# Performance work log

Hardware: AMD Instinct MI355X
Metric: run time of the kernel (lower is better)

## Reference

```python
import jax, jax.numpy as jnp
import numpy as np

B, S, D = 2, 4096, 768
H = 12
HD = D // H  # 64


def setup_inputs() -> dict:
    key = jax.random.key(0)
    ks = jax.random.split(key, 6)
    scale = 0.02
    return {
        "x": jax.random.normal(ks[0], (B, S, D), dtype=jnp.float32),
        "w_query": jax.random.normal(ks[1], (D, D), dtype=jnp.float32) * scale,
        "w_key": jax.random.normal(ks[2], (D, D), dtype=jnp.float32) * scale,
        "w_value": jax.random.normal(ks[3], (D, D), dtype=jnp.float32) * scale,
        "w_out": jax.random.normal(ks[4], (D, D), dtype=jnp.float32) * scale,
        "b_out": jax.random.normal(ks[5], (D,), dtype=jnp.float32) * scale,
    }


def reference(x, w_query, w_key, w_value, w_out, b_out):
    b, s, d = x.shape
    # Linear(in, out) applies x @ W.T; weights here stored as [out, in]-equivalent
    # square matrices, so use x @ W.T for parity with torch semantics.
    q = (x @ w_query.T).reshape(b, s, H, HD).transpose(0, 2, 1, 3)  # [b,h,s,hd]
    k = (x @ w_key.T).reshape(b, s, H, HD).transpose(0, 2, 1, 3)
    v = (x @ w_value.T).reshape(b, s, H, HD).transpose(0, 2, 1, 3)

    scores = jnp.einsum("bhqd,bhkd->bhqk", q, k)  # [b,h,s,s]
    causal = jnp.triu(jnp.ones((s, s), dtype=bool), k=1)
    scores = jnp.where(causal, -jnp.inf, scores)
    # original scales AFTER masking: softmax(masked / sqrt(head_dim))
    att = jax.nn.softmax(scores / jnp.sqrt(jnp.float32(HD)), axis=-1)
    # dropout p=0.0 (eval) -> identity
    ctx = jnp.einsum("bhqk,bhkd->bhqd", att, v)  # [b,h,s,hd]
    ctx = ctx.transpose(0, 2, 1, 3).reshape(b, s, d)
    return ctx @ w_out.T + b_out
```

## Files before the change

kernel.cpp:

```cpp
#include <hip/hip_runtime.h>
#include <stdint.h>

typedef unsigned short u16;
typedef __attribute__((ext_vector_type(8))) short bf16x8;
typedef __attribute__((ext_vector_type(4))) float f32x4;

#define MFMA(a,b,c) __builtin_amdgcn_mfma_f32_16x16x32_bf16((a),(b),(c),0,0,0)

static constexpr int S  = 4096;
static constexpr int D  = 768;
static constexpr int H  = 12;
static constexpr int HD = 64;

__device__ __forceinline__ u16 f2b(float f){
  union { float f; unsigned u; } v; v.f = f;
  unsigned r = (v.u + 0x7fffu + ((v.u >> 16) & 1u)) >> 16;
  return (u16)r;
}

__device__ __forceinline__ unsigned pack_bf16_trunc(float a, float b){
  return __builtin_amdgcn_perm(__float_as_uint(b), __float_as_uint(a), 0x07060302u);
}

__device__ __forceinline__ void cp16(const u16* g, u16* l){
  __builtin_amdgcn_global_load_lds(
      (const __attribute__((address_space(1))) unsigned int*)g,
      (__attribute__((address_space(3))) unsigned int*)l, 16, 0, 0);
}

__device__ __forceinline__ bf16x8 quad_transpose(unsigned M0, unsigned M1,
                                                 unsigned M2, unsigned M3){
  auto r0 = __builtin_amdgcn_permlane32_swap(M0, M2, false, false);
  auto r1 = __builtin_amdgcn_permlane32_swap(M1, M3, false, false);
  auto s0 = __builtin_amdgcn_permlane16_swap(r0[0], r0[1], false, false);
  auto s1 = __builtin_amdgcn_permlane16_swap(r1[0], r1[1], false, false);
  union { unsigned u[4]; bf16x8 v; } r;
  r.u[0] = s0[0];
  r.u[1] = s1[0];
  r.u[2] = s0[1];
  r.u[3] = s1[1];
  return r.v;
}

static constexpr int NX4 = (2 * S * D) / 4;
static constexpr int NW4 = (D * D) / 4;
__global__ void castall(const float* __restrict__ x,  const float* __restrict__ wq,
                        const float* __restrict__ wk, const float* __restrict__ wv,
                        const float* __restrict__ wo,
                        u16* __restrict__ xb,  u16* __restrict__ wqb,
                        u16* __restrict__ wkb, u16* __restrict__ wvb,
                        u16* __restrict__ wob){
  int i = blockIdx.x * 256 + threadIdx.x;
  const float* s; u16* d; int off;
  if (i < NX4) { s = x; d = xb; off = i; }
  else {
    int j = i - NX4; int wsel = j / NW4; off = j - wsel * NW4;
    if (wsel >= 4) return;
    s = (wsel == 0) ? wq : (wsel == 1) ? wk : (wsel == 2) ? wv : wo;
    d = (wsel == 0) ? wqb : (wsel == 1) ? wkb : (wsel == 2) ? wvb : wob;
  }
  float4 v = ((const float4*)s)[off];
  uint2 o;
  o.x = (unsigned)f2b(v.x) | ((unsigned)f2b(v.y) << 16);
  o.y = (unsigned)f2b(v.z) | ((unsigned)f2b(v.w) << 16);
  ((uint2*)d)[off] = o;
}

__global__ __launch_bounds__(256, 2) void qkv_gemm(
    const u16* __restrict__ xb, const u16* __restrict__ wq, const u16* __restrict__ wk,
    const u16* __restrict__ wv, u16* __restrict__ Qb, u16* __restrict__ Kb, u16* __restrict__ Vt)
{
  __shared__ __align__(16) u16 As[128 * 64];
  __shared__ __align__(16) u16 Bs[128 * 64];
  const int t = threadIdx.x;
  const int mblk = blockIdx.x, nblk = blockIdx.y, z = blockIdx.z;
  const u16* W = (z == 0) ? wq : (z == 1) ? wk : wv;
  const int w = t >> 6, lane = t & 63, quad = lane >> 4, l16 = lane & 15;
  const int wr = w >> 1, wc = w & 1;
  const int l7 = l16 & 7;

  f32x4 acc[4][4];
  #pragma unroll
  for (int i = 0; i < 4; i++)
    #pragma unroll
    for (int j = 0; j < 4; j++) acc[i][j] = (f32x4){0.f, 0.f, 0.f, 0.f};

  int srow[4], schk[4];
  #pragma unroll
  for (int i = 0; i < 4; i++) {
    int s = i * 256 + t;
    srow[i] = s >> 3;
    schk[i] = (s & 7) ^ (srow[i] & 7);
  }
  const u16* gA = xb + (size_t)(mblk * 128) * D;
  const u16* gB = W  + (size_t)(nblk * 128) * D;

  for (int k0 = 0; k0 < D; k0 += 64) {
    __syncthreads();
    #pragma unroll
    for (int i = 0; i < 4; i++) {
      int s = i * 256 + t;
      cp16(gA + (size_t)srow[i] * D + k0 + schk[i] * 8, As + s * 8);
      cp16(gB + (size_t)srow[i] * D + k0 + schk[i] * 8, Bs + s * 8);
    }
    __syncthreads();
    #pragma unroll
    for (int j = 0; j < 2; j++) {
      bf16x8 af[4], bfr[4];
      #pragma unroll
      for (int mt = 0; mt < 4; mt++)
        af[mt]  = *(const bf16x8*)(As + (wr * 64 + mt * 16 + l16) * 64 + ((j * 4 + quad) ^ l7) * 8);
      #pragma unroll
      for (int nt = 0; nt < 4; nt++)
        bfr[nt] = *(const bf16x8*)(Bs + (wc * 64 + nt * 16 + l16) * 64 + ((j * 4 + quad) ^ l7) * 8);
      #pragma unroll
      for (int mt = 0; mt < 4; mt++)
        #pragma unroll
        for (int nt = 0; nt < 4; nt++)
          acc[mt][nt] = MFMA(af[mt], bfr[nt], acc[mt][nt]);
    }
  }

  const float qscale = 0.18033688011112042f;
  #pragma unroll
  for (int mt = 0; mt < 4; mt++) {
    int m0 = mblk * 128 + wr * 64 + mt * 16 + quad * 4;
    #pragma unroll
    for (int nt = 0; nt < 4; nt++) {
      int n = nblk * 128 + wc * 64 + nt * 16 + l16;
      int h = n >> 6, hd = n & 63;
      if (z == 2) {
        int b = m0 >> 12, s0 = m0 & 4095;
        u16* p = Vt + (((size_t)(b * H + h) * HD + hd)) * S + s0;
        uint2 pk;
        pk.x = (unsigned)f2b(acc[mt][nt][0]) | ((unsigned)f2b(acc[mt][nt][1]) << 16);
        pk.y = (unsigned)f2b(acc[mt][nt][2]) | ((unsigned)f2b(acc[mt][nt][3]) << 16);
        *(uint2*)p = pk;
      } else {
        u16* dst = (z == 0) ? Qb : Kb;
        float sc = (z == 0) ? qscale : 1.0f;
        #pragma unroll
        for (int r = 0; r < 4; r++) {
          int m = m0 + r; int b = m >> 12, s = m & 4095;
          dst[((size_t)(b * H + h) * S + s) * HD + hd] = f2b(acc[mt][nt][r] * sc);
        }
      }
    }
  }
}

__global__ __launch_bounds__(256, 2) void attn(
    const u16* __restrict__ Qb, const u16* __restrict__ Kb,
    const u16* __restrict__ Vt, u16* __restrict__ ctx)
{
  __shared__ __align__(16) u16 Ks[128 * 64];
  __shared__ __align__(16) u16 Vts[64 * 128];
  __shared__ float Lbuf[2][2][16];
  const int t = threadIdx.x, w = t >> 6, lane = t & 63, quad = lane >> 4, l16 = lane & 15;
  const int l7 = l16 & 7;
  const int wq = w >> 1, wk = w & 1;

  const int p       = (int)blockIdx.x;
  const int bh      = p % 24;
  const int qtile64 = 63 - p / 24;
  const int q0   = qtile64 * 64;
  const int nt   = qtile64 / 2 + 1;
  const int doff = qtile64 & 1;

  const u16* Qh = Qb + (size_t)bh * S * HD;
  const u16* Kh = Kb + (size_t)bh * S * HD;
  const u16* Vh = Vt + (size_t)bh * S * HD;
  const int b = bh / H, h = bh % H;

  bf16x8 qf[2][2];
  #pragma unroll
  for (int qt = 0; qt < 2; qt++)
    #pragma unroll
    for (int ksh = 0; ksh < 2; ksh++)
      qf[qt][ksh] = *(const bf16x8*)(Qh + (size_t)(q0 + wq * 32 + qt * 16 + l16) * HD + ksh * 32 + quad * 8);

  f32x4 ao[2][4];
  #pragma unroll
  for (int qt = 0; qt < 2; qt++)
    #pragma unroll
    for (int co = 0; co < 4; co++) ao[qt][co] = (f32x4){0.f, 0.f, 0.f, 0.f};
  float lsum[2] = {0.f, 0.f};

  int krow[4], kchk[4], vrow[4], vchk[4];
  #pragma unroll
  for (int i = 0; i < 4; i++) {
    int s = i * 256 + t;
    krow[i] = s >> 3;  kchk[i] = (s & 7)  ^ (krow[i] & 7);
    vrow[i] = s >> 4;  vchk[i] = (s & 15) ^ (vrow[i] & 15);
  }

  for (int it = 0; it < nt; ++it) {
    const int kv0 = it * 128;
    const bool diag    = (it == nt - 1);
    const bool skipall = diag && (wk == 1) && (doff == 0);
    const bool mdiag   = diag && (wk == doff);

    __syncthreads();
    #pragma unroll
    for (int i = 0; i < 4; i++) {
      int s = i * 256 + t;
      cp16(Kh + (size_t)(kv0 + krow[i]) * HD + kchk[i] * 8, Ks + s * 8);
      cp16(Vh + (size_t)vrow[i] * S + kv0 + vchk[i] * 8,    Vts + s * 8);
    }
    __syncthreads();

    if (!skipall) {
      #pragma unroll
      for (int g = 0; g < 2; g++) {
        unsigned pA[2][2], pB[2][2];
        #pragma unroll
        for (int ktL = 0; ktL < 2; ktL++) {
          const int kt  = g * 2 + ktL;
          const int krw = wk * 64 + kt * 16 + l16;
          bf16x8 kf0 = *(const bf16x8*)(Ks + krw * 64 + ((0 + quad) ^ l7) * 8);
          bf16x8 kf1 = *(const bf16x8*)(Ks + krw * 64 + ((4 + quad) ^ l7) * 8);
          #pragma unroll
          for (int qt = 0; qt < 2; qt++) {
            f32x4 s0 = (f32x4){0.f, 0.f, 0.f, 0.f};
            s0 = MFMA(kf0, qf[qt][0], s0);
            s0 = MFMA(kf1, qf[qt][1], s0);
            if (mdiag) {
              const int qoff = wq * 32 + (qt - kt) * 16 + l16;
              #pragma unroll
              for (int r = 0; r < 4; r++)
                s0[r] = (quad * 4 + r > qoff) ? -1e30f : s0[r];
            }
            float p0 = __builtin_amdgcn_exp2f(s0[0]);
            float p1 = __builtin_amdgcn_exp2f(s0[1]);
            float p2 = __builtin_amdgcn_exp2f(s0[2]);
            float p3 = __builtin_amdgcn_exp2f(s0[3]);
            lsum[qt] += (p0 + p1) + (p2 + p3);
            pA[qt][ktL] = pack_bf16_trunc(p0, p1);
            pB[qt][ktL] = pack_bf16_trunc(p2, p3);
          }
        }
        bf16x8 pf[2];
        #pragma unroll
        for (int qt = 0; qt < 2; qt++)
          pf[qt] = quad_transpose(pA[qt][0], pB[qt][0], pA[qt][1], pB[qt][1]);
        #pragma unroll
        for (int co = 0; co < 4; co++) {
          const int vrw = co * 16 + l16;
          bf16x8 vf = *(const bf16x8*)(Vts + vrw * 128 + ((wk * 8 + g * 4 + quad) ^ (vrw & 15)) * 8);
          #pragma unroll
          for (int qt = 0; qt < 2; qt++)
            ao[qt][co] = MFMA(vf, pf[qt], ao[qt][co]);
        }
      }
    }
  }

  #pragma unroll
  for (int qt = 0; qt < 2; qt++) {
    float v = lsum[qt];
    v += __shfl_xor(v, 16, 64);
    v += __shfl_xor(v, 32, 64);
    lsum[qt] = v;
  }

  __syncthreads();
  float* red = wq ? (float*)Vts : (float*)Ks;
  if (wk == 1) {
    #pragma unroll
    for (int qt = 0; qt < 2; qt++)
      #pragma unroll
      for (int co = 0; co < 4; co++)
        *(f32x4*)(red + ((qt * 4 + co) * 64 + lane) * 4) = ao[qt][co];
    if (lane < 16) {
      #pragma unroll
      for (int qt = 0; qt < 2; qt++) Lbuf[wq][qt][lane] = lsum[qt];
    }
  }
  __syncthreads();
  if (wk == 0) {
    #pragma unroll
    for (int qt = 0; qt < 2; qt++) {
      float tot = lsum[qt] + Lbuf[wq][qt][l16];
      float inv = 1.0f / tot;
      int token = b * S + q0 + wq * 32 + qt * 16 + l16;
      #pragma unroll
      for (int co = 0; co < 4; co++) {
        f32x4 pr = *(const f32x4*)(red + ((qt * 4 + co) * 64 + lane) * 4);
        f32x4 sv = ao[qt][co] + pr;
        uint2 pk;
        pk.x = (unsigned)f2b(sv[0] * inv) | ((unsigned)f2b(sv[1] * inv) << 16);
        pk.y = (unsigned)f2b(sv[2] * inv) | ((unsigned)f2b(sv[3] * inv) << 16);
        *(uint2*)(ctx + (size_t)token * D + h * HD + co * 16 + quad * 4) = pk;
      }
    }
  }
}

__global__ __launch_bounds__(256, 2) void out_gemm(
    const u16* __restrict__ ctx, const u16* __restrict__ wo,
    const float* __restrict__ bias, float* __restrict__ out)
{
  __shared__ __align__(16) u16 As[128 * 64];
  __shared__ __align__(16) u16 Bs[128 * 64];
  const int t = threadIdx.x;
  const int mblk = blockIdx.x, nblk = blockIdx.y;
  const int w = t >> 6, lane = t & 63, quad = lane >> 4, l16 = lane & 15;
  const int wr = w >> 1, wc = w & 1;
  const int l7 = l16 & 7;

  f32x4 acc[4][4];
  #pragma unroll
  for (int i = 0; i < 4; i++)
    #pragma unroll
    for (int j = 0; j < 4; j++) acc[i][j] = (f32x4){0.f, 0.f, 0.f, 0.f};

  int srow[4], schk[4];
  #pragma unroll
  for (int i = 0; i < 4; i++) {
    int s = i * 256 + t;
    srow[i] = s >> 3;
    schk[i] = (s & 7) ^ (srow[i] & 7);
  }
  const u16* gA = ctx + (size_t)(mblk * 128) * D;
  const u16* gB = wo  + (size_t)(nblk * 128) * D;

  for (int k0 = 0; k0 < D; k0 += 64) {
    __syncthreads();
    #pragma unroll
    for (int i = 0; i < 4; i++) {
      int s = i * 256 + t;
      cp16(gA + (size_t)srow[i] * D + k0 + schk[i] * 8, As + s * 8);
      cp16(gB + (size_t)srow[i] * D + k0 + schk[i] * 8, Bs + s * 8);
    }
    __syncthreads();
    #pragma unroll
    for (int j = 0; j < 2; j++) {
      bf16x8 af[4], bfr[4];
      #pragma unroll
      for (int mt = 0; mt < 4; mt++)
        af[mt]  = *(const bf16x8*)(As + (wr * 64 + mt * 16 + l16) * 64 + ((j * 4 + quad) ^ l7) * 8);
      #pragma unroll
      for (int nt = 0; nt < 4; nt++)
        bfr[nt] = *(const bf16x8*)(Bs + (wc * 64 + nt * 16 + l16) * 64 + ((j * 4 + quad) ^ l7) * 8);
      #pragma unroll
      for (int mt = 0; mt < 4; mt++)
        #pragma unroll
        for (int nt = 0; nt < 4; nt++)
          acc[mt][nt] = MFMA(af[mt], bfr[nt], acc[mt][nt]);
    }
  }

  #pragma unroll
  for (int mt = 0; mt < 4; mt++) {
    int m0 = mblk * 128 + wr * 64 + mt * 16 + quad * 4;
    #pragma unroll
    for (int nt = 0; nt < 4; nt++) {
      int n = nblk * 128 + wc * 64 + nt * 16 + l16;
      float bv = bias[n];
      #pragma unroll
      for (int r = 0; r < 4; r++)
        out[(size_t)(m0 + r) * D + n] = acc[mt][nt][r] + bv;
    }
  }
}

extern "C" void kernel_launch(void* const* d_in, const int* in_sizes, int n_in,
                              void* d_out, int out_size, void* d_ws, size_t ws_size,
                              hipStream_t stream) {
  const float* x    = (const float*)d_in[0];
  const float* wq   = (const float*)d_in[1];
  const float* wk   = (const float*)d_in[2];
  const float* wv   = (const float*)d_in[3];
  const float* wo   = (const float*)d_in[4];
  const float* bo   = (const float*)d_in[5];
  float* out = (float*)d_out;

  u16* ws = (u16*)d_ws;
  const size_t NX = (size_t)2 * S * D;
  const size_t NW = (size_t)D * D;
  u16* xb  = ws;
  u16* wqb = ws + NX;
  u16* wkb = wqb + NW;
  u16* wvb = wkb + NW;
  u16* wob = wvb + NW;
  u16* Qb  = wob + NW;
  u16* Kb  = Qb + NX;
  u16* Vt  = Kb + NX;
  u16* ctx = xb;

  const int total4 = NX4 + 4 * NW4;
  castall<<<(total4 + 255) / 256, 256, 0, stream>>>(x, wq, wk, wv, wo, xb, wqb, wkb, wvb, wob);

  qkv_gemm<<<dim3(64, 6, 3), 256, 0, stream>>>(xb, wqb, wkb, wvb, Qb, Kb, Vt);
  attn<<<dim3(1536), 256, 0, stream>>>(Qb, Kb, Vt, ctx);
  out_gemm<<<dim3(64, 6), 256, 0, stream>>>(ctx, wob, bo, out);
}
```

Before: 214.6 us.

## Double-buffer 64-wide K/V tiles with async prefetch and MFMA priority hints

Splits each 128-key KV tile into two 64-key tiles held in a double-buffered LDS ring. The load of the next tile is issued before the current tile is computed, and raw s_waitcnt/s_barrier replace the paired __syncthreads. The aim is to hide global-memory latency behind MFMA work, and s_setprio is raised around the MFMA sections. The costs are twice as many iterations, each with less work, plus hand-written waitcnt counts that must match the compiler-emitted loads. The causal diagonal masking is also reworked for the 64-wide tiles.

```diff
diff --git a/kernel.cpp b/kernel.cpp
--- a/kernel.cpp
+++ b/kernel.cpp
@@ -153,8 +153,8 @@
     const u16* __restrict__ Qb, const u16* __restrict__ Kb,
     const u16* __restrict__ Vt, u16* __restrict__ ctx)
 {
-  __shared__ __align__(16) u16 Ks[128 * 64];
-  __shared__ __align__(16) u16 Vts[64 * 128];
+  __shared__ __align__(16) u16 Ks[2][64 * 64];
+  __shared__ __align__(16) u16 Vts[2][64 * 64];
   __shared__ float Lbuf[2][2][16];
   const int t = threadIdx.x, w = t >> 6, lane = t & 63, quad = lane >> 4, l16 = lane & 15;
   const int l7 = l16 & 7;
@@ -163,9 +163,8 @@
   const int p       = (int)blockIdx.x;
   const int bh      = p % 24;
   const int qtile64 = 63 - p / 24;
-  const int q0   = qtile64 * 64;
-  const int nt   = qtile64 / 2 + 1;
-  const int doff = qtile64 & 1;
+  const int q0 = qtile64 * 64;
+  const int nt = qtile64 + 1;
 
   const u16* Qh = Qb + (size_t)bh * S * HD;
   const u16* Kh = Kb + (size_t)bh * S * HD;
@@ -178,6 +177,7 @@
     #pragma unroll
     for (int ksh = 0; ksh < 2; ksh++)
       qf[qt][ksh] = *(const bf16x8*)(Qh + (size_t)(q0 + wq * 32 + qt * 16 + l16) * HD + ksh * 32 + quad * 8);
+  asm volatile("s_waitcnt vmcnt(0)" ::: "memory");
 
   f32x4 ao[2][4];
   #pragma unroll
@@ -186,73 +186,75 @@
     for (int co = 0; co < 4; co++) ao[qt][co] = (f32x4){0.f, 0.f, 0.f, 0.f};
   float lsum[2] = {0.f, 0.f};
 
-  int krow[4], kchk[4], vrow[4], vchk[4];
-  #pragma unroll
-  for (int i = 0; i < 4; i++) {
-    int s = i * 256 + t;
-    krow[i] = s >> 3;  kchk[i] = (s & 7)  ^ (krow[i] & 7);
-    vrow[i] = s >> 4;  vchk[i] = (s & 15) ^ (vrow[i] & 15);
-  }
+  const int r0 = t >> 3;
+  const int c0 = (t & 7) ^ (r0 & 7);
+
+  auto stage = [&](int kv, int d){
+    cp16(Kh + (size_t)(kv + r0)      * HD + c0 * 8, &Ks[d][0] + t * 8);
+    cp16(Kh + (size_t)(kv + r0 + 32) * HD + c0 * 8, &Ks[d][0] + (t + 256) * 8);
+    cp16(Vh + (size_t)r0 * S        + kv + c0 * 8, &Vts[d][0] + t * 8);
+    cp16(Vh + (size_t)(r0 + 32) * S + kv + c0 * 8, &Vts[d][0] + (t + 256) * 8);
+  };
+
+  stage(0, 0);
 
   for (int it = 0; it < nt; ++it) {
-    const int kv0 = it * 128;
-    const bool diag    = (it == nt - 1);
-    const bool skipall = diag && (wk == 1) && (doff == 0);
-    const bool mdiag   = diag && (wk == doff);
-
-    __syncthreads();
-    #pragma unroll
-    for (int i = 0; i < 4; i++) {
-      int s = i * 256 + t;
-      cp16(Kh + (size_t)(kv0 + krow[i]) * HD + kchk[i] * 8, Ks + s * 8);
-      cp16(Vh + (size_t)vrow[i] * S + kv0 + vchk[i] * 8,    Vts + s * 8);
-    }
-    __syncthreads();
+    const int cur = it & 1;
+    const bool diag = (it == nt - 1);
+    if (!diag) stage((it + 1) * 64, cur ^ 1);
+    if (!diag) asm volatile("s_waitcnt vmcnt(4)\ns_barrier" ::: "memory");
+    else       asm volatile("s_waitcnt vmcnt(0)\ns_barrier" ::: "memory");
+
+    const bool skipall = diag && (wk == 1) && (wq == 0);
+    const bool mdiag   = diag && (wk == wq);
 
     if (!skipall) {
-      #pragma unroll
-      for (int g = 0; g < 2; g++) {
-        unsigned pA[2][2], pB[2][2];
-        #pragma unroll
-        for (int ktL = 0; ktL < 2; ktL++) {
-          const int kt  = g * 2 + ktL;
-          const int krw = wk * 64 + kt * 16 + l16;
-          bf16x8 kf0 = *(const bf16x8*)(Ks + krw * 64 + ((0 + quad) ^ l7) * 8);
-          bf16x8 kf1 = *(const bf16x8*)(Ks + krw * 64 + ((4 + quad) ^ l7) * 8);
-          #pragma unroll
-          for (int qt = 0; qt < 2; qt++) {
-            f32x4 s0 = (f32x4){0.f, 0.f, 0.f, 0.f};
-            s0 = MFMA(kf0, qf[qt][0], s0);
-            s0 = MFMA(kf1, qf[qt][1], s0);
-            if (mdiag) {
-              const int qoff = wq * 32 + (qt - kt) * 16 + l16;
-              #pragma unroll
-              for (int r = 0; r < 4; r++)
-                s0[r] = (quad * 4 + r > qoff) ? -1e30f : s0[r];
-            }
-            float p0 = __builtin_amdgcn_exp2f(s0[0]);
-            float p1 = __builtin_amdgcn_exp2f(s0[1]);
-            float p2 = __builtin_amdgcn_exp2f(s0[2]);
-            float p3 = __builtin_amdgcn_exp2f(s0[3]);
-            lsum[qt] += (p0 + p1) + (p2 + p3);
-            pA[qt][ktL] = pack_bf16_trunc(p0, p1);
-            pB[qt][ktL] = pack_bf16_trunc(p2, p3);
+      const u16* Kc = &Ks[cur][0];
+      const u16* Vc = &Vts[cur][0];
+      unsigned pA[2][2], pB[2][2];
+      #pragma unroll
+      for (int ktL = 0; ktL < 2; ktL++) {
+        const int krw = wk * 32 + ktL * 16 + l16;
+        bf16x8 kf0 = *(const bf16x8*)(Kc + krw * 64 + ((0 + quad) ^ l7) * 8);
+        bf16x8 kf1 = *(const bf16x8*)(Kc + krw * 64 + ((4 + quad) ^ l7) * 8);
+        #pragma unroll
+        for (int qt = 0; qt < 2; qt++) {
+          f32x4 s0 = (f32x4){0.f, 0.f, 0.f, 0.f};
+          __builtin_amdgcn_s_setprio(1);
+          s0 = MFMA(kf0, qf[qt][0], s0);
+          s0 = MFMA(kf1, qf[qt][1], s0);
+          __builtin_amdgcn_s_setprio(0);
+          if (mdiag) {
+            const int qoff = (qt - ktL) * 16 + l16;
+            #pragma unroll
+            for (int r = 0; r < 4; r++)
+              s0[r] = (quad * 4 + r > qoff) ? -1e30f : s0[r];
           }
-        }
-        bf16x8 pf[2];
-        #pragma unroll
-        for (int qt = 0; qt < 2; qt++)
-          pf[qt] = quad_transpose(pA[qt][0], pB[qt][0], pA[qt][1], pB[qt][1]);
-        #pragma unroll
-        for (int co = 0; co < 4; co++) {
-          const int vrw = co * 16 + l16;
-          bf16x8 vf = *(const bf16x8*)(Vts + vrw * 128 + ((wk * 8 + g * 4 + quad) ^ (vrw & 15)) * 8);
-          #pragma unroll
-          for (int qt = 0; qt < 2; qt++)
-            ao[qt][co] = MFMA(vf, pf[qt], ao[qt][co]);
+          float p0 = __builtin_amdgcn_exp2f(s0[0]);
+          float p1 = __builtin_amdgcn_exp2f(s0[1]);
+          float p2 = __builtin_amdgcn_exp2f(s0[2]);
+          float p3 = __builtin_amdgcn_exp2f(s0[3]);
+          lsum[qt] += (p0 + p1) + (p2 + p3);
+          pA[qt][ktL] = pack_bf16_trunc(p0, p1);
+          pB[qt][ktL] = pack_bf16_trunc(p2, p3);
         }
       }
-    }
+      bf16x8 pf[2];
+      #pragma unroll
+      for (int qt = 0; qt < 2; qt++)
+        pf[qt] = quad_transpose(pA[qt][0], pB[qt][0], pA[qt][1], pB[qt][1]);
+      __builtin_amdgcn_s_setprio(1);
+      #pragma unroll
+      for (int co = 0; co < 4; co++) {
+        const int vrw = co * 16 + l16;
+        bf16x8 vf = *(const bf16x8*)(Vc + vrw * 64 + ((wk * 4 + quad) ^ (vrw & 7)) * 8);
+        #pragma unroll
+        for (int qt = 0; qt < 2; qt++)
+          ao[qt][co] = MFMA(vf, pf[qt], ao[qt][co]);
+      }
+      __builtin_amdgcn_s_setprio(0);
+    }
+    asm volatile("s_barrier" ::: "memory");
   }
 
   #pragma unroll
@@ -263,8 +265,7 @@
     lsum[qt] = v;
   }
 
-  __syncthreads();
-  float* red = wq ? (float*)Vts : (float*)Ks;
+  float* red = wq ? (float*)&Vts[0][0] : (float*)&Ks[0][0];
   if (wk == 1) {
     #pragma unroll
     for (int qt = 0; qt < 2; qt++)
```

New measurement: 211.8 us. No clear change (-1.3%).
